# Kernel optimization log

Measured on AMD Instinct MI355X. Metric: run time of the kernel, lower is better.

The kernel has to match this reference:

```python
import jax, jax.numpy as jnp
import numpy as np


def setup_inputs() -> dict:
    key = jax.random.key(0)
    k1, k2 = jax.random.split(key)
    B, N, M = 8, 8192, 8192
    source_points = jax.random.normal(k1, (B, N, 3), dtype=jnp.float32)
    target_points = jax.random.normal(k2, (B, M, 3), dtype=jnp.float32)
    return {"source_points": source_points, "target_points": target_points}


def reference(source_points, target_points):
    # dist: [B, N, M]  (same math as (x[:, :, None] - y[:, None]) ** 2 summed over coords)
    s_sq = jnp.sum(source_points ** 2, axis=-1)  # [B, N]
    t_sq = jnp.sum(target_points ** 2, axis=-1)  # [B, M]
    cross = jnp.einsum("bnd,bmd->bnm", source_points, target_points)  # [B, N, M]
    dist = s_sq[:, :, None] + t_sq[:, None, :] - 2.0 * cross
    min_s2t = jnp.min(dist, axis=2)  # [B, N] nearest target for each source point
    min_t2s = jnp.min(dist, axis=1)  # [B, M] nearest source for each target point
    chamfer = jnp.mean(min_s2t, axis=1) + jnp.mean(min_t2s, axis=1)  # [B]
    return chamfer
```

## Files before the change

### kernel.cpp

```cpp
#include <hip/hip_runtime.h>


typedef float f32x16 __attribute__((ext_vector_type(16)));
typedef short bf16x8 __attribute__((ext_vector_type(8)));

constexpr int BATCH  = 8;
constexpr int NPTS   = 8192;
constexpr int BLOCK  = 256;
constexpr int QTILE  = 256;
constexpr int QB     = NPTS / QTILE;
constexpr int DSPLIT = 2;
constexpr int DBR    = NPTS / DSPLIT;
constexpr int CH     = 256;
constexpr int NCH    = DBR / CH;

constexpr size_t FRAGB_N = (size_t)BATCH * NPTS * 2;
constexpr size_t WS1_N   = (size_t)DSPLIT * BATCH * NPTS * 8;
constexpr size_t TM_N    = (size_t)BATCH * NPTS;

static __device__ __forceinline__ float fmin3(float a, float b, float c) {
    return fminf(fminf(a, b), c);
}
static __device__ __forceinline__ unsigned short bf16h(float f) {
    unsigned int u = __float_as_uint(f);
    u += 0x7fffu + ((u >> 16) & 1u);
    return (unsigned short)(u >> 16);
}
static __device__ __forceinline__ float bf16tof(unsigned short h) {
    return __uint_as_float(((unsigned int)h) << 16);
}
static __device__ __forceinline__ unsigned int pack2(unsigned short a, unsigned short b) {
    return (unsigned int)a | ((unsigned int)b << 16);
}
static __device__ __forceinline__ float tree16(const f32x16& a) {
    float m = fmin3(a[0], a[1], a[2]);
    m = fmin3(m, a[3], a[4]);   m = fmin3(m, a[5], a[6]);
    m = fmin3(m, a[7], a[8]);   m = fmin3(m, a[9], a[10]);
    m = fmin3(m, a[11], a[12]); m = fmin3(m, a[13], a[14]);
    return fminf(m, a[15]);
}

__global__ __launch_bounds__(BLOCK) void chamfer_prep(
    const float* __restrict__ tgt, uint4* __restrict__ fragB,
    unsigned int* __restrict__ tmins, float* __restrict__ out)
{
    const int i = blockIdx.x * BLOCK + threadIdx.x;
    const float* tp = tgt + (size_t)i * 3;
    float px = tp[0], py = tp[1], pz = tp[2];
    float nx = -px, ny = -py, nz = -pz;
    float ht = 0.5f * fmaf(px, px, fmaf(py, py, pz * pz));
    const unsigned short one = bf16h(1.0f);
    unsigned short nxh = bf16h(nx), nxl = bf16h(nx - bf16tof(nxh));
    unsigned short nyh = bf16h(ny), nyl = bf16h(ny - bf16tof(nyh));
    unsigned short nzh = bf16h(nz), nzl = bf16h(nz - bf16tof(nzh));
    unsigned short hh = bf16h(ht),  hl = bf16h(ht - bf16tof(hh));
    fragB[2 * i + 0] = make_uint4(pack2(nxh, nxl), pack2(nxh, nyh),
                                  pack2(nyl, nyh), pack2(nzh, nzl));
    fragB[2 * i + 1] = make_uint4(pack2(nzh, one), pack2(one, hh),
                                  pack2(hl, 0), 0u);
    tmins[i] = 0x7f7f7f7fu;
    if (i < BATCH) out[i] = 0.0f;
}

__global__ __launch_bounds__(BLOCK) void chamfer_nn(
    const float* __restrict__ src, const uint4* __restrict__ fragB,
    float* __restrict__ ws1, unsigned int* __restrict__ tmins)
{
    __shared__ uint4 Bfr0[CH], Bfr1[CH];
    __shared__ int   sht[CH];

    const int tid  = threadIdx.x;
    const int lane = tid & 63;
    const int w    = tid >> 6;
    const int half = lane >> 5;
    const int l31  = lane & 31;
    const int qb   = blockIdx.x;
    const int b    = blockIdx.y;
    const int ds   = blockIdx.z;

    const unsigned short one = bf16h(1.0f);
    bf16x8 af0, af1;
#pragma unroll
    for (int g = 0; g < 2; g++) {
        const int q = qb * QTILE + w * 64 + g * 32 + l31;
        const float* qp = src + ((size_t)b * NPTS + q) * 3;
        float qx = qp[0], qy = qp[1], qz = qp[2];
        float hq = 0.5f * fmaf(qx, qx, fmaf(qy, qy, qz * qz));
        unsigned short xh = bf16h(qx), xl = bf16h(qx - bf16tof(xh));
        unsigned short yh = bf16h(qy), yl = bf16h(qy - bf16tof(yh));
        unsigned short zh = bf16h(qz), zl = bf16h(qz - bf16tof(zh));
        unsigned short qh = bf16h(hq), ql = bf16h(hq - bf16tof(qh));
        bf16x8 a;
        if (half == 0) {
            a[0] = (short)xh; a[1] = (short)xh; a[2] = (short)xl;
            a[3] = (short)yh; a[4] = (short)yh; a[5] = (short)yl;
            a[6] = (short)zh; a[7] = (short)zh;
        } else {
            a[0] = (short)zl; a[1] = (short)qh; a[2] = (short)ql;
            a[3] = (short)one; a[4] = (short)one;
            a[5] = 0; a[6] = 0; a[7] = 0;
        }
        if (g == 0) af0 = a; else af1 = a;
    }

    float rmn0[16], rmn1[16];
#pragma unroll
    for (int r = 0; r < 16; r++) { rmn0[r] = 3.4e38f; rmn1[r] = 3.4e38f; }
    const f32x16 zz = {};
    const uint4* Bh = half ? Bfr1 : Bfr0;

    const uint4* fb = fragB + ((size_t)b * NPTS + (size_t)ds * DBR) * 2;
    unsigned int* tm = tmins + (size_t)b * NPTS + (size_t)ds * DBR;

    uint4 r0 = fb[2 * tid + 0], r1 = fb[2 * tid + 1];

    for (int c = 0; c < NCH; ++c) {
        __syncthreads();
        if (c > 0) {
            float v = fmaxf(__int_as_float(sht[tid]), 0.0f);
            atomicMin(&tm[(c - 1) * CH + tid], __float_as_uint(v));
        }
        Bfr0[tid] = r0;
        Bfr1[tid] = r1;
        sht[tid] = 0x7f7f7f7f;
        __syncthreads();
        if (c + 1 < NCH) {
            r0 = fb[2 * (((c + 1) * CH) + tid) + 0];
            r1 = fb[2 * (((c + 1) * CH) + tid) + 1];
        }

#pragma unroll
        for (int tp = 0; tp < CH / 64; ++tp) {
            const int t0 = tp * 2, t1 = tp * 2 + 1;
            bf16x8 b0 = *reinterpret_cast<const bf16x8*>(&Bh[t0 * 32 + l31]);
            bf16x8 b1 = *reinterpret_cast<const bf16x8*>(&Bh[t1 * 32 + l31]);
            f32x16 a00 = __builtin_amdgcn_mfma_f32_32x32x16_bf16(af0, b0, zz, 0, 0, 0);
            f32x16 a01 = __builtin_amdgcn_mfma_f32_32x32x16_bf16(af0, b1, zz, 0, 0, 0);
            f32x16 a10 = __builtin_amdgcn_mfma_f32_32x32x16_bf16(af1, b0, zz, 0, 0, 0);
            f32x16 a11 = __builtin_amdgcn_mfma_f32_32x32x16_bf16(af1, b1, zz, 0, 0, 0);
#pragma unroll
            for (int r = 0; r < 16; r++) {
                rmn0[r] = fmin3(rmn0[r], a00[r], a01[r]);
                rmn1[r] = fmin3(rmn1[r], a10[r], a11[r]);
            }
            float c0 = fminf(tree16(a00), tree16(a10));
            float c1 = fminf(tree16(a01), tree16(a11));
            atomicMin(&sht[t0 * 32 + l31], __float_as_int(c0));
            atomicMin(&sht[t1 * 32 + l31], __float_as_int(c1));
        }
    }
    __syncthreads();
    {
        float v = fmaxf(__int_as_float(sht[tid]), 0.0f);
        atomicMin(&tm[(NCH - 1) * CH + tid], __float_as_uint(v));
    }

    float* w1 = ws1 + ((size_t)ds * BATCH + b) * NPTS * 8;
    const int qbase = qb * QTILE + w * 64;
#pragma unroll
    for (int r = 0; r < 16; r++) {
        float a = rmn0[r], bv = rmn1[r];
        a  = fminf(a,  __shfl_xor(a,  16, 64));
        bv = fminf(bv, __shfl_xor(bv, 16, 64));
        a  = fminf(a,  __shfl_xor(a,  8, 64));
        bv = fminf(bv, __shfl_xor(bv, 8, 64));
        if (l31 < 8) {
            const int row = (r & 3) + 8 * (r >> 2) + 4 * half;
            w1[(size_t)(qbase + row) * 8 + l31]      = a;
            w1[(size_t)(qbase + 32 + row) * 8 + l31] = bv;
        }
    }
}

__global__ __launch_bounds__(BLOCK) void chamfer_final(
    const float* __restrict__ ws1, const unsigned int* __restrict__ tmins,
    float* __restrict__ out)
{
    const int seg = blockIdx.x;
    const int b   = blockIdx.y;
    const int tid = threadIdx.x;
    float acc = 0.0f;

    if (seg < 16) {
#pragma unroll
        for (int rep = 0; rep < 2; rep++) {
            const int q = seg * 512 + rep * 256 + tid;
            float m = 3.4e38f;
#pragma unroll
            for (int d = 0; d < DSPLIT; d++) {
                const float4* p = (const float4*)(ws1 +
                    ((size_t)d * BATCH + b) * NPTS * 8 + (size_t)q * 8);
                float4 v0 = p[0], v1 = p[1];
                m = fmin3(m, v0.x, v0.y); m = fmin3(m, v0.z, v0.w);
                m = fmin3(m, v1.x, v1.y); m = fmin3(m, v1.z, v1.w);
            }
            acc += fmaxf(m, 0.0f);
        }
    } else {
#pragma unroll 8
        for (int k = 0; k < NPTS / BLOCK; k++)
            acc += __uint_as_float(tmins[(size_t)b * NPTS + k * BLOCK + tid]);
    }

    for (int off = 32; off > 0; off >>= 1) acc += __shfl_down(acc, off, 64);
    __shared__ float wsum[4];
    if ((tid & 63) == 0) wsum[tid >> 6] = acc;
    __syncthreads();
    if (tid == 0)
        atomicAdd(&out[b],
                  (wsum[0] + wsum[1] + wsum[2] + wsum[3]) * (2.0f / (float)NPTS));
}

extern "C" void kernel_launch(void* const* d_in, const int* in_sizes, int n_in,
                              void* d_out, int out_size, void* d_ws, size_t ws_size,
                              hipStream_t stream) {
    const float* src = (const float*)d_in[0];
    const float* tgt = (const float*)d_in[1];
    float* out = (float*)d_out;

    uint4* fragB        = (uint4*)d_ws;
    float* ws1          = (float*)(fragB + FRAGB_N);
    unsigned int* tmins = (unsigned int*)(ws1 + WS1_N);

    chamfer_prep<<<BATCH * NPTS / BLOCK, BLOCK, 0, stream>>>(tgt, fragB, tmins, out);
    chamfer_nn<<<dim3(QB, BATCH, DSPLIT), BLOCK, 0, stream>>>(src, fragB, ws1, tmins);
    chamfer_final<<<dim3(17, BATCH), BLOCK, 0, stream>>>(ws1, tmins, out);
}
```

Measured before the change: 106.7 us.

## Split database four ways and reduce source mins via global atomicMin

Raises the database split from 2 to 4, so the grid grows to 1024 blocks and each block handles fewer chunks, which should improve load balance and latency hiding. The per-row source minima are now fully reduced within the wave and written with global atomicMin into a compact array, replacing the 8-wide per-split workspace that the final kernel had to rescan. Target-min atomics are deferred to the end using a per-chunk shared array, which removes the per-chunk global atomic flush and one shared reset. The costs are more global atomics overall, more shared memory, and repeated source-point setup across the extra splits.

```diff
diff --git a/kernel.cpp b/kernel.cpp
--- a/kernel.cpp
+++ b/kernel.cpp
@@ -9,14 +9,13 @@
 constexpr int BLOCK  = 256;
 constexpr int QTILE  = 256;
 constexpr int QB     = NPTS / QTILE;
-constexpr int DSPLIT = 2;
+constexpr int DSPLIT = 4;
 constexpr int DBR    = NPTS / DSPLIT;
 constexpr int CH     = 256;
 constexpr int NCH    = DBR / CH;
 
 constexpr size_t FRAGB_N = (size_t)BATCH * NPTS * 2;
-constexpr size_t WS1_N   = (size_t)DSPLIT * BATCH * NPTS * 8;
-constexpr size_t TM_N    = (size_t)BATCH * NPTS;
+constexpr size_t SM_N    = (size_t)BATCH * NPTS;
 
 static __device__ __forceinline__ float fmin3(float a, float b, float c) {
     return fminf(fminf(a, b), c);
@@ -42,7 +41,8 @@
 
 __global__ __launch_bounds__(BLOCK) void chamfer_prep(
     const float* __restrict__ tgt, uint4* __restrict__ fragB,
-    unsigned int* __restrict__ tmins, float* __restrict__ out)
+    unsigned int* __restrict__ smins, unsigned int* __restrict__ tmins,
+    float* __restrict__ out)
 {
     const int i = blockIdx.x * BLOCK + threadIdx.x;
     const float* tp = tgt + (size_t)i * 3;
@@ -58,16 +58,17 @@
                                   pack2(nyl, nyh), pack2(nzh, nzl));
     fragB[2 * i + 1] = make_uint4(pack2(nzh, one), pack2(one, hh),
                                   pack2(hl, 0), 0u);
+    smins[i] = 0x7f7f7f7fu;
     tmins[i] = 0x7f7f7f7fu;
     if (i < BATCH) out[i] = 0.0f;
 }
 
 __global__ __launch_bounds__(BLOCK) void chamfer_nn(
     const float* __restrict__ src, const uint4* __restrict__ fragB,
-    float* __restrict__ ws1, unsigned int* __restrict__ tmins)
+    unsigned int* __restrict__ smins, unsigned int* __restrict__ tmins)
 {
     __shared__ uint4 Bfr0[CH], Bfr1[CH];
-    __shared__ int   sht[CH];
+    __shared__ int   sht[NCH][CH];
 
     const int tid  = threadIdx.x;
     const int lane = tid & 63;
@@ -77,6 +78,9 @@
     const int qb   = blockIdx.x;
     const int b    = blockIdx.y;
     const int ds   = blockIdx.z;
+
+#pragma unroll
+    for (int c = 0; c < NCH; c++) sht[c][tid] = 0x7f7f7f7f;
 
     const unsigned short one = bf16h(1.0f);
     bf16x8 af0, af1;
@@ -110,23 +114,17 @@
     const uint4* Bh = half ? Bfr1 : Bfr0;
 
     const uint4* fb = fragB + ((size_t)b * NPTS + (size_t)ds * DBR) * 2;
-    unsigned int* tm = tmins + (size_t)b * NPTS + (size_t)ds * DBR;
 
     uint4 r0 = fb[2 * tid + 0], r1 = fb[2 * tid + 1];
 
     for (int c = 0; c < NCH; ++c) {
         __syncthreads();
-        if (c > 0) {
-            float v = fmaxf(__int_as_float(sht[tid]), 0.0f);
-            atomicMin(&tm[(c - 1) * CH + tid], __float_as_uint(v));
-        }
         Bfr0[tid] = r0;
         Bfr1[tid] = r1;
-        sht[tid] = 0x7f7f7f7f;
         __syncthreads();
         if (c + 1 < NCH) {
-            r0 = fb[2 * (((c + 1) * CH) + tid) + 0];
-            r1 = fb[2 * (((c + 1) * CH) + tid) + 1];
+            r0 = fb[2 * ((c + 1) * CH + tid) + 0];
+            r1 = fb[2 * ((c + 1) * CH + tid) + 1];
         }
 
 #pragma unroll
@@ -145,63 +143,50 @@
             }
             float c0 = fminf(tree16(a00), tree16(a10));
             float c1 = fminf(tree16(a01), tree16(a11));
-            atomicMin(&sht[t0 * 32 + l31], __float_as_int(c0));
-            atomicMin(&sht[t1 * 32 + l31], __float_as_int(c1));
+            atomicMin(&sht[c][t0 * 32 + l31], __float_as_int(c0));
+            atomicMin(&sht[c][t1 * 32 + l31], __float_as_int(c1));
         }
     }
     __syncthreads();
-    {
-        float v = fmaxf(__int_as_float(sht[tid]), 0.0f);
-        atomicMin(&tm[(NCH - 1) * CH + tid], __float_as_uint(v));
-    }
-
-    float* w1 = ws1 + ((size_t)ds * BATCH + b) * NPTS * 8;
+
+    unsigned int* tm = tmins + (size_t)b * NPTS + (size_t)ds * DBR;
+#pragma unroll
+    for (int c = 0; c < NCH; c++) {
+        float v = fmaxf(__int_as_float(sht[c][tid]), 0.0f);
+        atomicMin(&tm[c * CH + tid], __float_as_uint(v));
+    }
+
+    unsigned int* sm = smins + (size_t)b * NPTS;
     const int qbase = qb * QTILE + w * 64;
 #pragma unroll
     for (int r = 0; r < 16; r++) {
         float a = rmn0[r], bv = rmn1[r];
-        a  = fminf(a,  __shfl_xor(a,  16, 64));
-        bv = fminf(bv, __shfl_xor(bv, 16, 64));
-        a  = fminf(a,  __shfl_xor(a,  8, 64));
-        bv = fminf(bv, __shfl_xor(bv, 8, 64));
-        if (l31 < 8) {
+#pragma unroll
+        for (int off = 16; off > 0; off >>= 1) {
+            a  = fminf(a,  __shfl_xor(a,  off, 64));
+            bv = fminf(bv, __shfl_xor(bv, off, 64));
+        }
+        if (l31 == 0) {
             const int row = (r & 3) + 8 * (r >> 2) + 4 * half;
-            w1[(size_t)(qbase + row) * 8 + l31]      = a;
-            w1[(size_t)(qbase + 32 + row) * 8 + l31] = bv;
+            atomicMin(&sm[qbase + row],      __float_as_uint(fmaxf(a,  0.0f)));
+            atomicMin(&sm[qbase + 32 + row], __float_as_uint(fmaxf(bv, 0.0f)));
         }
     }
 }
 
 __global__ __launch_bounds__(BLOCK) void chamfer_final(
-    const float* __restrict__ ws1, const unsigned int* __restrict__ tmins,
+    const unsigned int* __restrict__ smins, const unsigned int* __restrict__ tmins,
     float* __restrict__ out)
 {
     const int seg = blockIdx.x;
     const int b   = blockIdx.y;
     const int tid = threadIdx.x;
     float acc = 0.0f;
-
-    if (seg < 16) {
-#pragma unroll
-        for (int rep = 0; rep < 2; rep++) {
-            const int q = seg * 512 + rep * 256 + tid;
-            float m = 3.4e38f;
-#pragma unroll
-            for (int d = 0; d < DSPLIT; d++) {
-                const float4* p = (const float4*)(ws1 +
-                    ((size_t)d * BATCH + b) * NPTS * 8 + (size_t)q * 8);
-                float4 v0 = p[0], v1 = p[1];
-                m = fmin3(m, v0.x, v0.y); m = fmin3(m, v0.z, v0.w);
-                m = fmin3(m, v1.x, v1.y); m = fmin3(m, v1.z, v1.w);
-            }
-            acc += fmaxf(m, 0.0f);
-        }
-    } else {
-#pragma unroll 8
-        for (int k = 0; k < NPTS / BLOCK; k++)
-            acc += __uint_as_float(tmins[(size_t)b * NPTS + k * BLOCK + tid]);
-    }
-
+#pragma unroll
+    for (int k = 0; k < 8; k++) {
+        const size_t i = (size_t)b * NPTS + seg * 2048 + k * BLOCK + tid;
+        acc += __uint_as_float(smins[i]) + __uint_as_float(tmins[i]);
+    }
     for (int off = 32; off > 0; off >>= 1) acc += __shfl_down(acc, off, 64);
     __shared__ float wsum[4];
     if ((tid & 63) == 0) wsum[tid >> 6] = acc;
@@ -219,10 +204,10 @@
     float* out = (float*)d_out;
 
     uint4* fragB        = (uint4*)d_ws;
-    float* ws1          = (float*)(fragB + FRAGB_N);
-    unsigned int* tmins = (unsigned int*)(ws1 + WS1_N);
-
-    chamfer_prep<<<BATCH * NPTS / BLOCK, BLOCK, 0, stream>>>(tgt, fragB, tmins, out);
-    chamfer_nn<<<dim3(QB, BATCH, DSPLIT), BLOCK, 0, stream>>>(src, fragB, ws1, tmins);
-    chamfer_final<<<dim3(17, BATCH), BLOCK, 0, stream>>>(ws1, tmins, out);
-}
+    unsigned int* smins = (unsigned int*)(fragB + FRAGB_N);
+    unsigned int* tmins = smins + SM_N;
+
+    chamfer_prep<<<BATCH * NPTS / BLOCK, BLOCK, 0, stream>>>(tgt, fragB, smins, tmins, out);
+    chamfer_nn<<<dim3(QB, BATCH, DSPLIT), BLOCK, 0, stream>>>(src, fragB, smins, tmins);
+    chamfer_final<<<dim3(4, BATCH), BLOCK, 0, stream>>>(smins, tmins, out);
+}
```

New measurement: 106.2 us. Within noise of the previous version (-0.5%).
